# Performance work log

Measured on AMD Instinct MI355X. Metric: run time of the kernel, lower is better.

## Reference

```python
import jax, jax.numpy as jnp
import numpy as np

T = 2048      # tokens (flattened batch*seq)
HID = 2048    # hidden_size
H = 16        # num heads
D = HID // H  # head_dim = 128
EPS = 1e-5
THETA = 1000000.0


def setup_inputs() -> dict:
    key = jax.random.key(0)
    k0, k1, k2 = jax.random.split(key, 3)
    return {
        "hidden_states": jax.random.normal(k0, (T, HID), jnp.float32),
        "positions": jnp.arange(T, dtype=jnp.int32),
        "w_qkv": jax.random.normal(k1, (HID, 3 * HID), jnp.float32) * 0.02,
        "q_norm_w": jnp.ones((HID,), jnp.float32),
        "k_norm_w": jnp.ones((HID,), jnp.float32),
        "w_o": jax.random.normal(k2, (HID, HID), jnp.float32) * 0.02,
    }


def _rmsnorm(x, w):
    # RMSNorm over the full flat q/k vector (q_size / kv_size), as in forward_native
    var = jnp.mean(jnp.square(x.astype(jnp.float32)), axis=-1, keepdims=True)
    return (x.astype(jnp.float32) * jax.lax.rsqrt(var + EPS)).astype(x.dtype) * w


def _rope(x, positions):
    # NEOX-style rotary over full head_dim. x: [T, H, D]
    half = D // 2
    inv_freq = 1.0 / (THETA ** (jnp.arange(half, dtype=jnp.float32) / half))
    ang = positions.astype(jnp.float32)[:, None] * inv_freq  # [T, half]
    cos = jnp.cos(ang)[:, None, :]  # [T, 1, half]
    sin = jnp.sin(ang)[:, None, :]
    x1, x2 = x[..., :half], x[..., half:]
    return jnp.concatenate([x1 * cos - x2 * sin, x2 * cos + x1 * sin], axis=-1)


def reference(hidden_states, positions, w_qkv, q_norm_w, k_norm_w, w_o):
    qkv = hidden_states @ w_qkv                      # [T, 3*HID]
    q, k, v = jnp.split(qkv, [HID, 2 * HID], axis=-1)
    q = _rmsnorm(q, q_norm_w)
    k = _rmsnorm(k, k_norm_w)
    q = _rope(q.reshape(T, H, D), positions)
    k = _rope(k.reshape(T, H, D), positions)
    v = v.reshape(T, H, D)
    scale = D ** -0.5
    scores = jnp.einsum('qhd,khd->hqk', q, k) * scale   # [H, T, T]
    causal = jnp.tril(jnp.ones((T, T), bool))
    scores = jnp.where(causal[None], scores, jnp.finfo(scores.dtype).min)
    probs = jax.nn.softmax(scores, axis=-1)
    attn = jnp.einsum('hqk,khd->qhd', probs, v).reshape(T, HID)
    return attn @ w_o
```

## Files before the change

### kernel.cpp

```cpp
#include <hip/hip_runtime.h>
#include <hip/hip_bf16.h>

typedef __attribute__((ext_vector_type(8))) short bf16x8;
typedef __attribute__((ext_vector_type(4))) float f32x4;

__device__ inline unsigned short f2b(float x) {
  __hip_bfloat16 b = __float2bfloat16(x);
  return *reinterpret_cast<unsigned short*>(&b);
}
__device__ inline float b2f(unsigned short u) {
  return __bfloat162float(*reinterpret_cast<const __hip_bfloat16*>(&u));
}

#define GAS(p) ((const __attribute__((address_space(1))) void*)(p))
#define LAS(p) ((__attribute__((address_space(3))) void*)(p))

__global__ __launch_bounds__(256) void cast_f32_bf16(const float* __restrict__ X,
                                                     unsigned short* __restrict__ Y, int n4) {
  int i = blockIdx.x * 256 + threadIdx.x;
  if (i < n4) {
    float4 v = reinterpret_cast<const float4*>(X)[i];
    ushort4 o;
    o.x = f2b(v.x); o.y = f2b(v.y); o.z = f2b(v.z); o.w = f2b(v.w);
    reinterpret_cast<ushort4*>(Y)[i] = o;
  }
}

__global__ __launch_bounds__(256) void tcast(const float* __restrict__ W,
                                             unsigned short* __restrict__ Wt, int K, int N) {
  __shared__ float tile[32][33];
  int n0 = blockIdx.x * 32, k0 = blockIdx.y * 32;
  int tx = threadIdx.x & 31, ty = threadIdx.x >> 5;
#pragma unroll
  for (int i = 0; i < 32; i += 8)
    tile[ty + i][tx] = W[(size_t)(k0 + ty + i) * N + n0 + tx];
  __syncthreads();
#pragma unroll
  for (int i = 0; i < 32; i += 8)
    Wt[(size_t)(n0 + ty + i) * K + k0 + tx] = f2b(tile[tx][ty + i]);
}

__global__ __launch_bounds__(256) void vtrans(const float* __restrict__ qkv,
                                              unsigned short* __restrict__ Vt) {
  __shared__ unsigned short tile[32][33];
  int c0 = blockIdx.x * 32;
  int t0 = blockIdx.y * 32;
  int tx = threadIdx.x & 31, ty = threadIdx.x >> 5;
#pragma unroll
  for (int i = 0; i < 32; i += 8)
    tile[ty + i][tx] = f2b(qkv[(size_t)(t0 + ty + i) * 6144 + 4096 + c0 + tx]);
  __syncthreads();
#pragma unroll
  for (int i = 0; i < 32; i += 8)
    Vt[(size_t)(c0 + ty + i) * 2048 + t0 + tx] = tile[tx][ty + i];
}

__global__ __launch_bounds__(256) void gemm_bt(const unsigned short* __restrict__ A,
                                               const unsigned short* __restrict__ Bt,
                                               float* __restrict__ C, int M, int N, int K) {
  __shared__ unsigned short As[128 * 32];
  __shared__ unsigned short Bs[128 * 32];
  const int tid = threadIdx.x;
  const int w = tid >> 6, l = tid & 63;
  const int lr = l & 15, lg = l >> 4;
  const int wm = (w >> 1) << 6, wn = (w & 1) << 6;
  const size_t bm = (size_t)blockIdx.y * 128, bn = (size_t)blockIdx.x * 128;

  const int srow = tid >> 2;
  const int scol = (tid & 3) << 3;
  const unsigned short* Ag = A + (bm + srow) * (size_t)K + scol;
  const unsigned short* Bg = Bt + (bn + srow) * (size_t)K + scol;
  unsigned short* Al = As + w * 512;
  unsigned short* Bl = Bs + w * 512;

  f32x4 acc[4][4] = {};

  for (int k0 = 0; k0 < K; k0 += 32) {
    __syncthreads();
    __builtin_amdgcn_global_load_lds(GAS(Ag + k0), LAS(Al), 16, 0, 0);
    __builtin_amdgcn_global_load_lds(GAS(Ag + (size_t)64 * K + k0), LAS(Al + 2048), 16, 0, 0);
    __builtin_amdgcn_global_load_lds(GAS(Bg + k0), LAS(Bl), 16, 0, 0);
    __builtin_amdgcn_global_load_lds(GAS(Bg + (size_t)64 * K + k0), LAS(Bl + 2048), 16, 0, 0);
    __syncthreads();

    bf16x8 af[4], bfr[4];
#pragma unroll
    for (int mi = 0; mi < 4; ++mi)
      af[mi] = *reinterpret_cast<const bf16x8*>(&As[(wm + mi * 16 + lr) * 32 + lg * 8]);
#pragma unroll
    for (int ni = 0; ni < 4; ++ni)
      bfr[ni] = *reinterpret_cast<const bf16x8*>(&Bs[(wn + ni * 16 + lr) * 32 + lg * 8]);
#pragma unroll
    for (int mi = 0; mi < 4; ++mi)
#pragma unroll
      for (int ni = 0; ni < 4; ++ni)
        acc[mi][ni] = __builtin_amdgcn_mfma_f32_16x16x32_bf16(af[mi], bfr[ni], acc[mi][ni], 0, 0, 0);
  }

#pragma unroll
  for (int mi = 0; mi < 4; ++mi)
#pragma unroll
    for (int ni = 0; ni < 4; ++ni)
#pragma unroll
      for (int r = 0; r < 4; ++r) {
        size_t row = bm + wm + mi * 16 + lg * 4 + r;
        size_t col = bn + wn + ni * 16 + lr;
        C[row * N + col] = acc[mi][ni][r];
      }
}

__global__ __launch_bounds__(256) void rms_rope(const float* __restrict__ qkv,
                                                const int* __restrict__ pos,
                                                const float* __restrict__ qw,
                                                const float* __restrict__ kw,
                                                unsigned short* __restrict__ qb,
                                                unsigned short* __restrict__ kb) {
  const int t = blockIdx.x;
  const float* row = qkv + (size_t)t * 6144;
  __shared__ float redq[4], redk[4];
  __shared__ float cs[64], sn[64];
  const int tid = threadIdx.x, w = tid >> 6, l = tid & 63;

  float sq = 0.f, sk = 0.f;
#pragma unroll
  for (int i = 0; i < 8; ++i) {
    float a = row[tid + i * 256]; sq += a * a;
    float b = row[2048 + tid + i * 256]; sk += b * b;
  }
#pragma unroll
  for (int m = 32; m >= 1; m >>= 1) { sq += __shfl_xor(sq, m, 64); sk += __shfl_xor(sk, m, 64); }
  if (l == 0) { redq[w] = sq; redk[w] = sk; }
  if (tid < 64) {
    float fr = exp2f(-(float)tid * 0.31143075889569016f);
    float ang = (float)pos[t] * fr;
    cs[tid] = cosf(ang);
    sn[tid] = sinf(ang);
  }
  __syncthreads();
  float rq = rsqrtf((redq[0] + redq[1] + redq[2] + redq[3]) * (1.f / 2048.f) + 1e-5f);
  float rk = rsqrtf((redk[0] + redk[1] + redk[2] + redk[3]) * (1.f / 2048.f) + 1e-5f);
  const float rqs = rq * 0.12753102543609887f;

  unsigned short* qo = qb + (size_t)t * 2048;
  unsigned short* ko = kb + (size_t)t * 2048;
#pragma unroll
  for (int pp = 0; pp < 4; ++pp) {
    int pr = tid + pp * 256;
    int h = pr >> 6, j = pr & 63;
    int b0 = h * 128 + j;
    float c = cs[j], s = sn[j];
    float x1 = row[b0] * rqs * qw[b0];
    float x2 = row[b0 + 64] * rqs * qw[b0 + 64];
    qo[b0]      = f2b(x1 * c - x2 * s);
    qo[b0 + 64] = f2b(x2 * c + x1 * s);
    float y1 = row[2048 + b0] * rk * kw[b0];
    float y2 = row[2048 + b0 + 64] * rk * kw[b0 + 64];
    ko[b0]      = f2b(y1 * c - y2 * s);
    ko[b0 + 64] = f2b(y2 * c + y1 * s);
  }
}

__device__ __forceinline__ void stage_kv(const unsigned short* __restrict__ kb_h,
                                         const unsigned short* __restrict__ vt_h,
                                         int k0, int w, int l,
                                         unsigned short* Ks, unsigned short* Vs) {
  const int r0 = l >> 4, cph = l & 15;
#pragma unroll
  for (int rb = 0; rb < 16; rb += 4) {
    int row = w * 16 + rb + r0;
    int clog = (cph & 8) | ((cph & 7) ^ (row & 7));
    const unsigned short* src = kb_h + (size_t)(k0 + row) * 2048 + clog * 8;
    __builtin_amdgcn_global_load_lds(GAS(src), LAS((char*)Ks + (w * 16 + rb) * 256), 16, 0, 0);
  }
  const int r0v = l >> 3, cpv = l & 7;
#pragma unroll
  for (int rb = 0; rb < 32; rb += 8) {
    int row = w * 32 + rb + r0v;
    int clog = cpv ^ (row & 7);
    const unsigned short* src = vt_h + (size_t)row * 2048 + k0 + clog * 8;
    __builtin_amdgcn_global_load_lds(GAS(src), LAS((char*)Vs + (w * 32 + rb) * 128), 16, 0, 0);
  }
}

template <bool MASKED>
__device__ __forceinline__ void attn_tile(int k0, int qrbase, int lr, int lg,
                                          const bf16x8 (&qf)[4],
                                          const unsigned short* __restrict__ Ks,
                                          const unsigned short* __restrict__ Vs,
                                          unsigned short* __restrict__ PsW,
                                          f32x4 (&oacc)[8], float (&mrow)[4], float (&lrow)[4]) {
  f32x4 s[4] = {};
  __builtin_amdgcn_s_setprio(1);
#pragma unroll
  for (int kc = 0; kc < 4; ++kc)
#pragma unroll
    for (int cg = 0; cg < 4; ++cg) {
      int key = cg * 16 + lr;
      int c = 4 * kc + lg;
      int cswz = (c & 8) | ((c & 7) ^ (key & 7));
      bf16x8 kf = *reinterpret_cast<const bf16x8*>(&Ks[key * 128 + cswz * 8]);
      s[cg] = __builtin_amdgcn_mfma_f32_16x16x32_bf16(qf[kc], kf, s[cg], 0, 0, 0);
    }
  __builtin_amdgcn_s_setprio(0);

#pragma unroll
  for (int r = 0; r < 4; ++r) {
    const int qr = qrbase + lg * 4 + r;
    float p0 = s[0][r], p1 = s[1][r], p2 = s[2][r], p3 = s[3][r];
    if (MASKED) {
      if (k0 + lr > qr)      p0 = -1e30f;
      if (k0 + 16 + lr > qr) p1 = -1e30f;
      if (k0 + 32 + lr > qr) p2 = -1e30f;
      if (k0 + 48 + lr > qr) p3 = -1e30f;
    }
    float mx = fmaxf(fmaxf(p0, p1), fmaxf(p2, p3));
#pragma unroll
    for (int m = 8; m >= 1; m >>= 1) mx = fmaxf(mx, __shfl_xor(mx, m, 16));
    float mnew = fmaxf(mrow[r], mx);
    float corr = exp2f(mrow[r] - mnew);
    p0 = exp2f(p0 - mnew); p1 = exp2f(p1 - mnew);
    p2 = exp2f(p2 - mnew); p3 = exp2f(p3 - mnew);
    lrow[r] = lrow[r] * corr + ((p0 + p1) + (p2 + p3));
    mrow[r] = mnew;
#pragma unroll
    for (int ni = 0; ni < 8; ++ni) oacc[ni][r] *= corr;
    const int prow = (lg * 4 + r) * 72;
    PsW[prow + lr]      = f2b(p0);
    PsW[prow + 16 + lr] = f2b(p1);
    PsW[prow + 32 + lr] = f2b(p2);
    PsW[prow + 48 + lr] = f2b(p3);
  }

  __builtin_amdgcn_s_setprio(1);
#pragma unroll
  for (int ks = 0; ks < 2; ++ks) {
    bf16x8 pf = *reinterpret_cast<const bf16x8*>(&PsW[lr * 72 + ks * 32 + lg * 8]);
#pragma unroll
    for (int ni = 0; ni < 8; ++ni) {
      int d = ni * 16 + lr;
      int c = ks * 4 + lg;
      int cswz = c ^ (d & 7);
      bf16x8 vf = *reinterpret_cast<const bf16x8*>(&Vs[d * 64 + cswz * 8]);
      oacc[ni] = __builtin_amdgcn_mfma_f32_16x16x32_bf16(pf, vf, oacc[ni], 0, 0, 0);
    }
  }
  __builtin_amdgcn_s_setprio(0);
}

__global__ __launch_bounds__(256) void attn_part(const unsigned short* __restrict__ qb,
                                                 const unsigned short* __restrict__ kb,
                                                 const unsigned short* __restrict__ vt,
                                                 unsigned short* __restrict__ Op,
                                                 float* __restrict__ ml) {
  __shared__ unsigned short Ks[2][64 * 128];
  __shared__ unsigned short Vs[2][128 * 64];
  __shared__ unsigned short Ps[4][16 * 72];
  const int p = blockIdx.x;
  const int xcd = p & 7;
  const int i = p >> 3;
  const int h = (xcd << 1) | (i & 1);
  const int j = i >> 1;
  const int qt = 31 - (j & 31);
  const int sp = j >> 5;
  const int q0 = qt * 64;
  const int kbeg = sp * 512;
  if (kbeg >= q0 + 64) return;
  const int kend = min(kbeg + 512, q0 + 64);
  const int nt = (kend - kbeg) >> 6;
  const int tid = threadIdx.x, w = tid >> 6, l = tid & 63;
  const int lr = l & 15, lg = l >> 4;
  const int qrbase = q0 + w * 16;

  const unsigned short* kb_h = kb + h * 128;
  const unsigned short* vt_h = vt + (size_t)h * 128 * 2048;

  stage_kv(kb_h, vt_h, kbeg, w, l, Ks[0], Vs[0]);

  bf16x8 qf[4];
  {
    const unsigned short* qp = qb + (size_t)(qrbase + lr) * 2048 + h * 128;
#pragma unroll
    for (int kc = 0; kc < 4; ++kc)
      qf[kc] = *reinterpret_cast<const bf16x8*>(qp + kc * 32 + lg * 8);
  }
  f32x4 oacc[8] = {};
  float mrow[4], lrow[4];
#pragma unroll
  for (int r = 0; r < 4; ++r) { mrow[r] = -1e30f; lrow[r] = 0.f; }

  __syncthreads();

  for (int t = 0; t < nt; ++t) {
    const int k0 = kbeg + t * 64;
    if (t + 1 < nt)
      stage_kv(kb_h, vt_h, k0 + 64, w, l, Ks[(t + 1) & 1], Vs[(t + 1) & 1]);
    if (k0 == q0)
      attn_tile<true>(k0, qrbase, lr, lg, qf, Ks[t & 1], Vs[t & 1], Ps[w], oacc, mrow, lrow);
    else
      attn_tile<false>(k0, qrbase, lr, lg, qf, Ks[t & 1], Vs[t & 1], Ps[w], oacc, mrow, lrow);
    __syncthreads();
  }

#pragma unroll
  for (int r = 0; r < 4; ++r)
#pragma unroll
    for (int m = 8; m >= 1; m >>= 1) lrow[r] += __shfl_xor(lrow[r], m, 16);

  const size_t base = (((size_t)sp * 16 + h) * 32 + qt) * 64;
#pragma unroll
  for (int ni = 0; ni < 8; ++ni)
#pragma unroll
    for (int r = 0; r < 4; ++r)
      Op[(base + w * 16 + lg * 4 + r) * 128 + ni * 16 + lr] = f2b(oacc[ni][r]);
  if (lr == 0) {
#pragma unroll
    for (int r = 0; r < 4; ++r) {
      size_t mi = (base + w * 16 + lg * 4 + r) * 2;
      ml[mi] = mrow[r]; ml[mi + 1] = lrow[r];
    }
  }
}

__global__ __launch_bounds__(256) void attn_combine(const unsigned short* __restrict__ Op,
                                                    const float* __restrict__ ml,
                                                    unsigned short* __restrict__ ob) {
  const int qt = blockIdx.x, h = blockIdx.y;
  const int q0 = qt * 64;
  const int ns = (qt >> 3) + 1;
  const int t = threadIdx.x;
  const int row = t >> 2, dp = (t & 3) * 32;

  float m_s[4], l_s[4];
  float M = -1e30f;
#pragma unroll
  for (int s = 0; s < 4; ++s) {
    if (s < ns) {
      size_t mi = ((((size_t)s * 16 + h) * 32 + qt) * 64 + row) * 2;
      m_s[s] = ml[mi]; l_s[s] = ml[mi + 1];
    } else { m_s[s] = -1e30f; l_s[s] = 0.f; }
    M = fmaxf(M, m_s[s]);
  }
  float L = 0.f, wgt[4];
#pragma unroll
  for (int s = 0; s < 4; ++s) { wgt[s] = exp2f(m_s[s] - M); L += l_s[s] * wgt[s]; }
  float invL = 1.f / L;

  float acc[32];
#pragma unroll
  for (int jj = 0; jj < 32; ++jj) acc[jj] = 0.f;
#pragma unroll
  for (int s = 0; s < 4; ++s) {
    if (s < ns) {
      const unsigned short* op = Op + ((((size_t)s * 16 + h) * 32 + qt) * 64 + row) * 128 + dp;
      float wg = wgt[s] * invL;
#pragma unroll
      for (int jj = 0; jj < 32; jj += 8) {
        bf16x8 v = *reinterpret_cast<const bf16x8*>(op + jj);
#pragma unroll
        for (int e = 0; e < 8; ++e) acc[jj + e] += wg * b2f((unsigned short)v[e]);
      }
    }
  }
  unsigned short* o = ob + (size_t)(q0 + row) * 2048 + h * 128 + dp;
#pragma unroll
  for (int jj = 0; jj < 32; ++jj) o[jj] = f2b(acc[jj]);
}

extern "C" void kernel_launch(void* const* d_in, const int* in_sizes, int n_in,
                              void* d_out, int out_size, void* d_ws, size_t ws_size,
                              hipStream_t stream) {
  const float* hs   = (const float*)d_in[0];
  const int*   pos  = (const int*)d_in[1];
  const float* wqkv = (const float*)d_in[2];
  const float* qnw  = (const float*)d_in[3];
  const float* knw  = (const float*)d_in[4];
  const float* wo   = (const float*)d_in[5];
  float* out = (float*)d_out;

  char* ws = (char*)d_ws;
  size_t off = 0;
  auto take = [&](size_t bytes) {
    char* p = ws + off;
    off = (off + bytes + 255) & ~(size_t)255;
    return p;
  };
  unsigned short* hidA  = (unsigned short*)take(2048ull * 2048 * 2);
  unsigned short* wqkvT = (unsigned short*)take(6144ull * 2048 * 2);
  unsigned short* woT   = (unsigned short*)take(2048ull * 2048 * 2);
  float*          qkvF  = (float*)take(2048ull * 6144 * 4);
  unsigned short* qbv   = (unsigned short*)take(2048ull * 2048 * 2);
  unsigned short* kbv   = (unsigned short*)take(2048ull * 2048 * 2);
  unsigned short* vtb   = (unsigned short*)take(2048ull * 2048 * 2);
  unsigned short* attnb = (unsigned short*)take(2048ull * 2048 * 2);
  unsigned short* Opart = (unsigned short*)qkvF;
  float*          mlb   = (float*)((char*)qkvF + 32ull * 1024 * 1024);

  cast_f32_bf16<<<4096, 256, 0, stream>>>(hs, hidA, 1048576);
  tcast<<<dim3(192, 64), 256, 0, stream>>>(wqkv, wqkvT, 2048, 6144);
  tcast<<<dim3(64, 64), 256, 0, stream>>>(wo, woT, 2048, 2048);
  gemm_bt<<<dim3(48, 16), 256, 0, stream>>>(hidA, wqkvT, qkvF, 2048, 6144, 2048);
  rms_rope<<<2048, 256, 0, stream>>>(qkvF, pos, qnw, knw, qbv, kbv);
  vtrans<<<dim3(64, 64), 256, 0, stream>>>(qkvF, vtb);
  attn_part<<<dim3(2048), 256, 0, stream>>>(qbv, kbv, vtb, Opart, mlb);
  attn_combine<<<dim3(32, 16), 256, 0, stream>>>(Opart, mlb, attnb);
  gemm_bt<<<dim3(16, 16), 256, 0, stream>>>(attnb, woT, out, 2048, 2048, 2048);
}
```

Measured before the change: 337.2 us.

## Add 256x256-tile triple-buffered GEMM with direct global-to-LDS loads for QKV projection

Adds a new GEMM kernel for the QKV projection. It uses 256x256 block tiles, 512 threads, three LDS buffers filled by global_load_lds, an XOR swizzle to avoid bank conflicts, and raised wave priority around the MFMA block. The goal is more data reuse per tile and overlap of global loads with compute compared with the older 128-tile kernel. The cost is 96KB of LDS per block and a grid of only 192 blocks, which may underfill the CUs.

```diff
diff --git a/kernel.cpp b/kernel.cpp
--- a/kernel.cpp
+++ b/kernel.cpp
@@ -99,6 +99,89 @@
 
 #pragma unroll
   for (int mi = 0; mi < 4; ++mi)
+#pragma unroll
+    for (int ni = 0; ni < 4; ++ni)
+#pragma unroll
+      for (int r = 0; r < 4; ++r) {
+        size_t row = bm + wm + mi * 16 + lg * 4 + r;
+        size_t col = bn + wn + ni * 16 + lr;
+        C[row * N + col] = acc[mi][ni][r];
+      }
+}
+
+__global__ __launch_bounds__(512, 2) void gemm256(const unsigned short* __restrict__ A,
+                                                  const unsigned short* __restrict__ Bt,
+                                                  float* __restrict__ C, int M, int N, int K) {
+  extern __shared__ unsigned short lds[];
+  const int tid = threadIdx.x, w = tid >> 6, l = tid & 63;
+  const int lr = l & 15, lg = (l >> 4) & 3;
+  const int wm = (w >> 2) * 128, wn = (w & 3) * 64;
+  const size_t bm = (size_t)blockIdx.y * 256, bn = (size_t)blockIdx.x * 256;
+  const int nt = K >> 5;
+
+  const int sr = w * 8 + (l >> 3);
+  const int sc = (l & 7) ^ (sr & 7);
+  const int sh = sc >> 2, sq = sc & 3;
+
+  auto stage = [&](int t) {
+    const int b = t % 3;
+    unsigned short* Ab = lds + (size_t)b * 16384;
+    unsigned short* Bb = Ab + 8192;
+    const int k0 = t * 32;
+#pragma unroll
+    for (int cc = 0; cc < 2; ++cc) {
+      const int r = cc * 64 + sr;
+      const int ccf = (cc * 64) & 0;
+      (void)ccf;
+      const unsigned short* sa = A + (bm + 2 * r + sh) * (size_t)K + k0 + sq * 8;
+      __builtin_amdgcn_global_load_lds(GAS(sa), LAS(Ab + (cc * 64 + w * 8) * 64), 16, 0, 0);
+      const unsigned short* sb = Bt + (bn + 2 * r + sh) * (size_t)K + k0 + sq * 8;
+      __builtin_amdgcn_global_load_lds(GAS(sb), LAS(Bb + (cc * 64 + w * 8) * 64), 16, 0, 0);
+    }
+  };
+
+  f32x4 acc[8][4] = {};
+
+  stage(0);
+  stage(1);
+
+  for (int t = 0; t < nt; ++t) {
+    if (t == nt - 1) asm volatile("s_waitcnt vmcnt(0)" ::: "memory");
+    else             asm volatile("s_waitcnt vmcnt(4)" ::: "memory");
+    __builtin_amdgcn_s_barrier();
+    if (t + 2 < nt) stage(t + 2);
+
+    const int b = t % 3;
+    const unsigned short* Ab = lds + (size_t)b * 16384;
+    const unsigned short* Bb = Ab + 8192;
+
+    bf16x8 af[8], bg[4];
+#pragma unroll
+    for (int mi = 0; mi < 8; ++mi) {
+      const int tr = wm + mi * 16 + lr;
+      const int r = tr >> 1;
+      const int p = (((tr & 1) << 2) + lg) ^ (r & 7);
+      af[mi] = *reinterpret_cast<const bf16x8*>(Ab + r * 64 + p * 8);
+    }
+#pragma unroll
+    for (int ni = 0; ni < 4; ++ni) {
+      const int tc = wn + ni * 16 + lr;
+      const int r = tc >> 1;
+      const int p = (((tc & 1) << 2) + lg) ^ (r & 7);
+      bg[ni] = *reinterpret_cast<const bf16x8*>(Bb + r * 64 + p * 8);
+    }
+
+    __builtin_amdgcn_s_setprio(1);
+#pragma unroll
+    for (int mi = 0; mi < 8; ++mi)
+#pragma unroll
+      for (int ni = 0; ni < 4; ++ni)
+        acc[mi][ni] = __builtin_amdgcn_mfma_f32_16x16x32_bf16(af[mi], bg[ni], acc[mi][ni], 0, 0, 0);
+    __builtin_amdgcn_s_setprio(0);
+  }
+
+#pragma unroll
+  for (int mi = 0; mi < 8; ++mi)
 #pragma unroll
     for (int ni = 0; ni < 4; ++ni)
 #pragma unroll
@@ -395,10 +478,12 @@
   unsigned short* Opart = (unsigned short*)qkvF;
   float*          mlb   = (float*)((char*)qkvF + 32ull * 1024 * 1024);
 
+  hipFuncSetAttribute((const void*)gemm256, hipFuncAttributeMaxDynamicSharedMemorySize, 98304);
+
   cast_f32_bf16<<<4096, 256, 0, stream>>>(hs, hidA, 1048576);
   tcast<<<dim3(192, 64), 256, 0, stream>>>(wqkv, wqkvT, 2048, 6144);
   tcast<<<dim3(64, 64), 256, 0, stream>>>(wo, woT, 2048, 2048);
-  gemm_bt<<<dim3(48, 16), 256, 0, stream>>>(hidA, wqkvT, qkvF, 2048, 6144, 2048);
+  gemm256<<<dim3(24, 8), 512, 98304, stream>>>(hidA, wqkvT, qkvF, 2048, 6144, 2048);
   rms_rope<<<2048, 256, 0, stream>>>(qkvF, pos, qnw, knw, qbv, kbv);
   vtrans<<<dim3(64, 64), 256, 0, stream>>>(qkvF, vtb);
   attn_part<<<dim3(2048), 256, 0, stream>>>(qbv, kbv, vtb, Opart, mlb);
```

Result: faster. 325.9 us (-3.4%).
